# Kernel optimization log

Hardware: AMD Instinct MI355X
Metric: run time of the kernel (lower is better)

## Reference

```python
import jax, jax.numpy as jnp
import numpy as np

S_LEN, BATCH, HID, HEADS = 2048, 4, 1024, 16
HD = HID // HEADS


def setup_inputs() -> dict:
    key = jax.random.key(0)
    ks = jax.random.split(key, 6)

    def lin_w(k, out_dim, in_dim):
        return jax.random.normal(k, (out_dim, in_dim), jnp.float32) * (1.0 / np.sqrt(in_dim))

    return {
        "hidden_states": jax.random.normal(ks[0], (S_LEN, BATCH, HID), jnp.float32),
        "Wq": lin_w(ks[1], HID, HID), "bq": jnp.zeros((HID,), jnp.float32),
        "Wk": lin_w(ks[2], HID, HID), "bk": jnp.zeros((HID,), jnp.float32),
        "Wv": lin_w(ks[3], HID, HID), "bv": jnp.zeros((HID,), jnp.float32),
        "Wf": lin_w(ks[4], HEADS, HID), "bf": jnp.zeros((HEADS,), jnp.float32),
        "Wo": lin_w(ks[5], HID, HID), "bo": jnp.zeros((HID,), jnp.float32),
    }


def _forget_attention(hidden_states, Wq, bq, Wk, bk, Wv, bv, Wf, bf, Wo, bo):
    S, B, H = hidden_states.shape
    nh, hd = HEADS, HD

    def shape(x):
        return x.reshape(S, B, nh, hd)

    q = shape(hidden_states @ Wq.T + bq)
    k = shape(hidden_states @ Wk.T + bk)
    v = shape(hidden_states @ Wv.T + bv)

    # kernel_fn = elu(x) + 1
    phi_q = jax.nn.elu(q) + 1.0
    phi_k = jax.nn.elu(k) + 1.0

    f = jax.nn.sigmoid(hidden_states @ Wf.T + bf)  # [S, B, nh]

    # F_{t,j} = prod_{i=j+1}^{t} f_i  factorizes into the recurrence:
    #   S_t = f_t * S_{t-1} + phi_k_t (x) v_t ;  z_t = f_t * z_{t-1} + phi_k_t
    # out_t = (phi_q_t . S_t) / (phi_q_t . z_t + eps)
    def step(carry, xs):
        Sm, z = carry                      # [B,nh,hd,hd], [B,nh,hd]
        ft, pk, pq, vt = xs                # [B,nh], [B,nh,hd] x3
        fte = ft[..., None]
        Sm = fte[..., None] * Sm + pk[..., :, None] * vt[..., None, :]
        z = fte * z + pk
        num = jnp.einsum('bhd,bhde->bhe', pq, Sm)
        den = jnp.einsum('bhd,bhd->bh', pq, z)[..., None]
        return (Sm, z), num / (den + 1e-6)

    init = (jnp.zeros((B, nh, hd, hd), hidden_states.dtype),
            jnp.zeros((B, nh, hd), hidden_states.dtype))
    _, out = jax.lax.scan(step, init, (f, phi_k, phi_q, v))

    out = out.reshape(S, B, H) @ Wo.T + bo
    return out, f


def reference(hidden_states, Wq, bq, Wk, bk, Wv, bv, Wf, bf, Wo, bo):
    out, f = _forget_attention(hidden_states, Wq, bq, Wk, bk, Wv, bv, Wf, bf, Wo, bo)
    return (out, jnp.zeros_like(out), f)
```

## Files before the change

### kernel.cpp

```cpp
#include <hip/hip_runtime.h>
#include <hip/hip_bf16.h>
#include <math.h>

#define S_LEN 2048
#define BATCH 4
#define HID   1024
#define HEADS 16
#define HD    64
#define SB    (S_LEN*BATCH)
#define CHUNK 64
#define NCHUNK (S_LEN/CHUNK)
#define BH    (BATCH*HEADS)
#define NSTK  3200

typedef __bf16 bf16x8 __attribute__((ext_vector_type(8)));
typedef float  f32x4  __attribute__((ext_vector_type(4)));
typedef unsigned short ushort_t;
typedef unsigned short u16x8 __attribute__((ext_vector_type(8)));
typedef unsigned short u16x4 __attribute__((ext_vector_type(4)));

__device__ __forceinline__ unsigned short f2bf(float x) {
    union { float f; unsigned int u; } un; un.f = x;
    unsigned int u = un.u;
    unsigned int r = (u + 0x7FFFu + ((u >> 16) & 1u)) >> 16;
    return (unsigned short)r;
}
__device__ __forceinline__ float bf2f(unsigned short s) {
    union { unsigned int u; float f; } un; un.u = ((unsigned int)s) << 16;
    return un.f;
}

#define JSW(row, j) ((j) ^ ((((row) >> 3) & 7) << 3))

#define GLL16(src, dst) __builtin_amdgcn_global_load_lds( \
    (const __attribute__((address_space(1))) void*)(src), \
    (__attribute__((address_space(3))) void*)(dst), 16, 0, 0)

#define NXU (SB*HID/4)
#define NW1 (NSTK*HID/4)
#define NW2 (HID*HID/4)
#define NBU (NSTK/4)
#define NTOT (NXU+NW1+NW2+NBU)

__global__ __launch_bounds__(256) void prep_kernel(
    const float* __restrict__ X,  const float* __restrict__ Wq,
    const float* __restrict__ Wk, const float* __restrict__ Wv,
    const float* __restrict__ Wf, const float* __restrict__ Wo,
    const float* __restrict__ bq, const float* __restrict__ bk,
    const float* __restrict__ bv, const float* __restrict__ bf,
    ushort_t* __restrict__ Xb, ushort_t* __restrict__ Wstk,
    ushort_t* __restrict__ Wob, float* __restrict__ bstk)
{
    const int i = blockIdx.x * 256 + threadIdx.x;
    if (i < NXU) {
        float4 v = ((const float4*)X)[i];
        ushort4 o; o.x=f2bf(v.x); o.y=f2bf(v.y); o.z=f2bf(v.z); o.w=f2bf(v.w);
        ((ushort4*)Xb)[i] = o;
    } else if (i < NXU + NW1) {
        const int idx4 = (i - NXU) * 4;
        const int row = idx4 >> 10, col = idx4 & 1023;
        float4 v;
        if      (row < 1024) v = *(const float4*)(Wq + (size_t)row*HID + col);
        else if (row < 2048) v = *(const float4*)(Wk + (size_t)(row-1024)*HID + col);
        else if (row < 3072) v = *(const float4*)(Wv + (size_t)(row-2048)*HID + col);
        else if (row < 3088) v = *(const float4*)(Wf + (size_t)(row-3072)*HID + col);
        else                 v = make_float4(0.f,0.f,0.f,0.f);
        ushort4 o; o.x=f2bf(v.x); o.y=f2bf(v.y); o.z=f2bf(v.z); o.w=f2bf(v.w);
        *(ushort4*)(Wstk + idx4) = o;
    } else if (i < NXU + NW1 + NW2) {
        const int idx4 = (i - NXU - NW1) * 4;
        float4 v = *(const float4*)(Wo + idx4);
        ushort4 o; o.x=f2bf(v.x); o.y=f2bf(v.y); o.z=f2bf(v.z); o.w=f2bf(v.w);
        *(ushort4*)(Wob + idx4) = o;
    } else if (i < NTOT) {
        const int idx4 = (i - NXU - NW1 - NW2) * 4;
        #pragma unroll
        for (int t = 0; t < 4; ++t) {
            const int c = idx4 + t;
            float v;
            if      (c < 1024) v = bq[c];
            else if (c < 2048) v = bk[c-1024];
            else if (c < 3072) v = bv[c-2048];
            else if (c < 3088) v = bf[c-3072];
            else               v = 0.f;
            bstk[c] = v;
        }
    }
}

__global__ __launch_bounds__(256) void qkvf_gemm(
    const ushort_t* __restrict__ X, const ushort_t* __restrict__ W,
    const float* __restrict__ bias,
    ushort_t* __restrict__ Q, ushort_t* __restrict__ Kr,
    ushort_t* __restrict__ V,
    float* __restrict__ f_out, float* __restrict__ logf_out)
{
    __shared__ ushort_t As[128 * 32];
    __shared__ ushort_t Bs[128 * 32];

    const int tid  = threadIdx.x;
    const int wave = tid >> 6, lane = tid & 63;
    const int waveM = wave >> 1, waveN = wave & 1;
    const int rowBase = blockIdx.x * 128;
    const int colBase = blockIdx.y * 128;
    const int K = HID;

    f32x4 acc[4][4];
    #pragma unroll
    for (int i = 0; i < 4; ++i)
        #pragma unroll
        for (int j = 0; j < 4; ++j)
            acc[i][j] = (f32x4){0.f, 0.f, 0.f, 0.f};

    const int srow = lane >> 2;
    const int scol = (lane & 3) * 8;

    const ushort_t* gA0 = X + (size_t)(rowBase + wave*16 + srow) * K + scol;
    const ushort_t* gB0 = W + (size_t)(colBase + wave*16 + srow) * K + scol;
    ushort_t* lA = As + (wave*16)*32;
    ushort_t* lB = Bs + (wave*16)*32;

    const int fr = lane & 15;
    const int fk = (lane >> 4) * 8;

    for (int k0 = 0; k0 < K; k0 += 32) {
        GLL16(gA0 + k0,                lA);
        GLL16(gA0 + (size_t)64*K + k0, lA + 64*32);
        GLL16(gB0 + k0,                lB);
        GLL16(gB0 + (size_t)64*K + k0, lB + 64*32);

        __syncthreads();

        bf16x8 a[4], b[4];
        #pragma unroll
        for (int i = 0; i < 4; ++i)
            a[i] = *(const bf16x8*)(As + (waveM*64 + i*16 + fr)*32 + fk);
        #pragma unroll
        for (int j = 0; j < 4; ++j)
            b[j] = *(const bf16x8*)(Bs + (waveN*64 + j*16 + fr)*32 + fk);

        #pragma unroll
        for (int i = 0; i < 4; ++i)
            #pragma unroll
            for (int j = 0; j < 4; ++j)
                acc[i][j] = __builtin_amdgcn_mfma_f32_16x16x32_bf16(
                    a[i], b[j], acc[i][j], 0, 0, 0);

        __syncthreads();
    }

    const int er = (lane >> 4) * 4;
    const int ec = lane & 15;
    #pragma unroll
    for (int i = 0; i < 4; ++i) {
        #pragma unroll
        for (int j = 0; j < 4; ++j) {
            const int r0 = rowBase + waveM*64 + i*16 + er;
            const int c0 = colBase + waveN*64 + j*16;
            if (c0 >= 3088) continue;
            const int c  = c0 + ec;
            const float bv = bias[c];
            #pragma unroll
            for (int k = 0; k < 4; ++k) {
                float v = acc[i][j][k] + bv;
                const int r = r0 + k;
                if (c0 < 1024) {
                    v = (v > 0.f) ? (v + 1.f) : __expf(v);
                    Q[(size_t)r * HID + c] = f2bf(v);
                } else if (c0 < 2048) {
                    v = (v > 0.f) ? (v + 1.f) : __expf(v);
                    Kr[(size_t)r * HID + (c - 1024)] = f2bf(v);
                } else if (c0 < 3072) {
                    V[(size_t)r * HID + (c - 2048)] = f2bf(v);
                } else {
                    const int n = c - 3072;
                    const float fv = 1.f / (1.f + __expf(-v));
                    f_out[(size_t)r * HEADS + n]    = fv;
                    logf_out[(size_t)r * HEADS + n] = -__logf(1.f + __expf(-v));
                }
            }
        }
    }
}

__global__ __launch_bounds__(256) void gemm_out(
    const ushort_t* __restrict__ X, const ushort_t* __restrict__ W,
    const float* __restrict__ bias, float* __restrict__ Y)
{
    __shared__ ushort_t As[128 * 32];
    __shared__ ushort_t Bs[128 * 32];

    const int tid  = threadIdx.x;
    const int wave = tid >> 6, lane = tid & 63;
    const int waveM = wave >> 1, waveN = wave & 1;
    const int rowBase = blockIdx.x * 128;
    const int colBase = blockIdx.y * 128;
    const int K = HID, N = HID;

    f32x4 acc[4][4];
    #pragma unroll
    for (int i = 0; i < 4; ++i)
        #pragma unroll
        for (int j = 0; j < 4; ++j)
            acc[i][j] = (f32x4){0.f, 0.f, 0.f, 0.f};

    const int srow = lane >> 2;
    const int scol = (lane & 3) * 8;

    const ushort_t* gA0 = X + (size_t)(rowBase + wave*16 + srow) * K + scol;
    const ushort_t* gB0 = W + (size_t)(colBase + wave*16 + srow) * K + scol;
    ushort_t* lA = As + (wave*16)*32;
    ushort_t* lB = Bs + (wave*16)*32;

    const int fr = lane & 15;
    const int fk = (lane >> 4) * 8;

    for (int k0 = 0; k0 < K; k0 += 32) {
        GLL16(gA0 + k0,                lA);
        GLL16(gA0 + (size_t)64*K + k0, lA + 64*32);
        GLL16(gB0 + k0,                lB);
        GLL16(gB0 + (size_t)64*K + k0, lB + 64*32);

        __syncthreads();

        bf16x8 a[4], b[4];
        #pragma unroll
        for (int i = 0; i < 4; ++i)
            a[i] = *(const bf16x8*)(As + (waveM*64 + i*16 + fr)*32 + fk);
        #pragma unroll
        for (int j = 0; j < 4; ++j)
            b[j] = *(const bf16x8*)(Bs + (waveN*64 + j*16 + fr)*32 + fk);

        #pragma unroll
        for (int i = 0; i < 4; ++i)
            #pragma unroll
            for (int j = 0; j < 4; ++j)
                acc[i][j] = __builtin_amdgcn_mfma_f32_16x16x32_bf16(
                    a[i], b[j], acc[i][j], 0, 0, 0);

        __syncthreads();
    }

    const int er = (lane >> 4) * 4;
    const int ec = lane & 15;
    #pragma unroll
    for (int i = 0; i < 4; ++i) {
        #pragma unroll
        for (int j = 0; j < 4; ++j) {
            const int r0 = rowBase + waveM*64 + i*16 + er;
            const int c  = colBase + waveN*64 + j*16 + ec;
            const float bv = bias[c];
            #pragma unroll
            for (int k = 0; k < 4; ++k) {
                const size_t off = (size_t)(r0 + k) * N + c;
                Y[off] = acc[i][j][k] + bv;
            }
        }
    }
}

__global__ __launch_bounds__(256) void pass1_kernel(
    const ushort_t* __restrict__ Kp, const ushort_t* __restrict__ Vp,
    const float* __restrict__ logf,
    ushort_t* __restrict__ Schunk, float* __restrict__ zchunk,
    float* __restrict__ Dchunk)
{
    __shared__ __align__(16) char smem[18688];
    ushort_t* vsT = (ushort_t*)smem;
    ushort_t* kTd = (ushort_t*)(smem + 9216);
    float*    exd = (float*)(smem + 18432);

    const int chunk = blockIdx.x;
    const int bh = blockIdx.y;
    const int b = bh >> 4, h = bh & 15;
    const int tid = threadIdx.x;
    const int wv = tid >> 6, ln = tid & 63;
    const int fr = ln & 15, q4 = ln >> 4;
    const size_t slot = (size_t)bh * NCHUNK + chunk;

    u16x8 vreg[2], kreg[2];
    #pragma unroll
    for (int it = 0; it < 2; ++it) {
        const int u = it*256 + tid;
        const int j = u >> 3, d8 = (u & 7) * 8;
        const size_t base = (size_t)((chunk*64 + j)*BATCH + b)*HID + h*HD + d8;
        vreg[it] = *(const u16x8*)(Vp + base);
        kreg[it] = *(const u16x8*)(Kp + base);
    }
    if (tid < 64) {
        float v = logf[(size_t)((chunk*64 + tid)*BATCH + b) * HEADS + h];
        #pragma unroll
        for (int off = 1; off < 64; off <<= 1) {
            float n = __shfl_up(v, off);
            if (tid >= off) v += n;
        }
        const float tot = __shfl(v, 63);
        exd[tid] = __expf(tot - v);
        if (tid == 63) Dchunk[slot] = __expf(tot);
    }
    __syncthreads();

    #pragma unroll
    for (int it = 0; it < 2; ++it) {
        const int u = it*256 + tid;
        const int j = u >> 3, d8 = (u & 7) * 8;
        const int js = j ^ ((u & 7) << 3);
        const float ex = exd[j];
        #pragma unroll
        for (int i = 0; i < 8; ++i) {
            vsT[(d8+i)*72 + js] = vreg[it][i];
            kTd[(d8+i)*72 + js] = f2bf(bf2f(kreg[it][i]) * ex);
        }
    }
    __syncthreads();

    f32x4 acc[4];
    #pragma unroll
    for (int nt = 0; nt < 4; ++nt) acc[nt] = (f32x4){0.f,0.f,0.f,0.f};
    #pragma unroll
    for (int k0 = 0; k0 < 64; k0 += 32) {
        const int rA = wv*16 + fr;
        bf16x8 av = *(const bf16x8*)(vsT + rA*72 + JSW(rA, k0 + q4*8));
        #pragma unroll
        for (int nt = 0; nt < 4; ++nt) {
            const int rB = nt*16 + fr;
            bf16x8 bk = *(const bf16x8*)(kTd + rB*72 + JSW(rB, k0 + q4*8));
            acc[nt] = __builtin_amdgcn_mfma_f32_16x16x32_bf16(av, bk, acc[nt], 0, 0, 0);
        }
    }

    if (wv == 0) {
        u16x8 onesu;
        #pragma unroll
        for (int i = 0; i < 8; ++i) onesu[i] = 0x3F80;
        const bf16x8 ones = *(const bf16x8*)&onesu;
        f32x4 zacc[4];
        #pragma unroll
        for (int nt = 0; nt < 4; ++nt) zacc[nt] = (f32x4){0.f,0.f,0.f,0.f};
        #pragma unroll
        for (int k0 = 0; k0 < 64; k0 += 32) {
            #pragma unroll
            for (int nt = 0; nt < 4; ++nt) {
                const int rB = nt*16 + fr;
                bf16x8 bk = *(const bf16x8*)(kTd + rB*72 + JSW(rB, k0 + q4*8));
                zacc[nt] = __builtin_amdgcn_mfma_f32_16x16x32_bf16(ones, bk, zacc[nt], 0, 0, 0);
            }
        }
        if (q4 == 0) {
            #pragma unroll
            for (int nt = 0; nt < 4; ++nt)
                zchunk[slot*64 + nt*16 + fr] = zacc[nt][0];
        }
    }

    ushort_t* sp = Schunk + slot * 4096;
    #pragma unroll
    for (int nt = 0; nt < 4; ++nt) {
        #pragma unroll
        for (int r = 0; r < 4; ++r) {
            const int e = wv*16 + q4*4 + r;
            sp[e*64 + nt*16 + fr] = f2bf(acc[nt][r]);
        }
    }
}

__global__ __launch_bounds__(128) void pass2_kernel(
    ushort_t* __restrict__ Schunk, float* __restrict__ zchunk,
    const float* __restrict__ Dchunk)
{
    __shared__ float Ds[NCHUNK];
    const int bh  = blockIdx.x >> 3;
    const int sl  = blockIdx.x & 7;
    const int tid = threadIdx.x;

    if (tid < NCHUNK) Ds[tid] = Dchunk[bh * NCHUNK + tid];

    float Sprev[4] = {0.f, 0.f, 0.f, 0.f};
    float zprev = 0.f;

    const size_t base  = (size_t)bh * NCHUNK * 4096 + sl * 512 + tid * 4;
    const size_t zbase = (size_t)bh * NCHUNK * 64;
    const bool doZ = (sl == 0) && (tid < 64);

    u16x4 b0 = *(const u16x4*)(Schunk + base);
    u16x4 b1 = *(const u16x4*)(Schunk + base + 4096);
    float z0v = 0.f, z1v = 0.f;
    if (doZ) {
        z0v = zchunk[zbase + tid];
        z1v = zchunk[zbase + 64 + tid];
    }
    __syncthreads();

    for (int c = 0; c < NCHUNK; ++c) {
        const float D = Ds[c];
        ushort_t* sp = Schunk + base + (size_t)c * 4096;
        u16x4 wout;
        #pragma unroll
        for (int i = 0; i < 4; ++i) {
            wout[i] = f2bf(Sprev[i]);
            Sprev[i] = D * Sprev[i] + bf2f(b0[i]);
        }
        *(u16x4*)sp = wout;
        b0 = b1;
        if (doZ) {
            zchunk[zbase + (size_t)c * 64 + tid] = zprev;
            zprev = D * zprev + z0v;
            z0v = z1v;
        }
        if (c + 2 < NCHUNK) {
            b1 = *(const u16x4*)(Schunk + base + (size_t)(c+2)*4096);
            if (doZ) z1v = zchunk[zbase + (size_t)(c+2)*64 + tid];
        }
    }
}

__global__ __launch_bounds__(256) void pass3_kernel(
    const ushort_t* __restrict__ Qp, const ushort_t* __restrict__ Kp,
    const ushort_t* __restrict__ Vp, const float* __restrict__ logf,
    const ushort_t* __restrict__ S0, const float* __restrict__ z0,
    ushort_t* __restrict__ AO)
{
    __shared__ __align__(16) char smem[28928];
    ushort_t* qs  = (ushort_t*)smem;
    ushort_t* ks  = (ushort_t*)(smem + 9216);
    ushort_t* vsT = (ushort_t*)(smem + 9216);
    ushort_t* psA = (ushort_t*)(smem + 18432);
    float* cc  = (float*)(smem + 27648);
    float* exT = (float*)(smem + 27904);
    float* qz  = (float*)(smem + 28160);
    float* den = (float*)(smem + 28416);
    float* zz  = (float*)(smem + 28672);

    const int chunk = blockIdx.x;
    const int bh = blockIdx.y;
    const int b = bh >> 4, h = bh & 15;
    const int tid = threadIdx.x;
    const int wv = tid >> 6, ln = tid & 63;
    const int fr = ln & 15, q4 = ln >> 4;
    const size_t slot = (size_t)bh * NCHUNK + chunk;

    u16x8 vreg[2];
    #pragma unroll
    for (int it = 0; it < 2; ++it) {
        const int u = it*256 + tid;
        const int j = u >> 3, d8 = (u & 7) * 8;
        vreg[it] = *(const u16x8*)(Vp + (size_t)((chunk*64 + j)*BATCH + b)*HID + h*HD + d8);
    }

    if (tid < 64) {
        zz[tid] = z0[slot * 64 + tid];
        float v = logf[(size_t)((chunk*64 + tid)*BATCH + b) * HEADS + h];
        #pragma unroll
        for (int off = 1; off < 64; off <<= 1) {
            float n = __shfl_up(v, off);
            if (tid >= off) v += n;
        }
        cc[tid]  = v;
        exT[tid] = __expf(v);
    }
    #pragma unroll
    for (int it = 0; it < 2; ++it) {
        const int u = it*256 + tid;
        const int r = u >> 3, c8 = (u & 7) * 8;
        const size_t goff = (size_t)((chunk*64 + r)*BATCH + b) * HID + h*HD + c8;
        *(u16x8*)(qs + r*72 + c8) = *(const u16x8*)(Qp + goff);
        *(u16x8*)(ks + r*72 + c8) = *(const u16x8*)(Kp + goff);
    }
    __syncthreads();

    f32x4 pacc[4];
    #pragma unroll
    for (int nt = 0; nt < 4; ++nt) pacc[nt] = (f32x4){0.f,0.f,0.f,0.f};
    #pragma unroll
    for (int k0 = 0; k0 < 64; k0 += 32) {
        bf16x8 af = *(const bf16x8*)(qs + (wv*16 + fr)*72 + k0 + q4*8);
        #pragma unroll
        for (int nt = 0; nt < 4; ++nt) {
            bf16x8 bfr = *(const bf16x8*)(ks + (nt*16 + fr)*72 + k0 + q4*8);
            pacc[nt] = __builtin_amdgcn_mfma_f32_16x16x32_bf16(af, bfr, pacc[nt], 0, 0, 0);
        }
    }
    {
        const int t = wv*16 + fr;
        const int d0 = q4 * 16;
        float s = 0.f;
        #pragma unroll
        for (int i = 0; i < 16; ++i)
            s += bf2f(qs[t*72 + d0 + i]) * zz[d0 + i];
        s += __shfl_xor(s, 16);
        s += __shfl_xor(s, 32);
        if (q4 == 0) qz[t] = s;
    }
    __syncthreads();

    #pragma unroll
    for (int it = 0; it < 2; ++it) {
        const int u = it*256 + tid;
        const int j = u >> 3, d8 = (u & 7) * 8;
        const int js = j ^ ((u & 7) << 3);
        #pragma unroll
        for (int i = 0; i < 8; ++i)
            vsT[(d8+i)*72 + js] = vreg[it][i];
    }
    {
        float rs[4] = {0.f, 0.f, 0.f, 0.f};
        float cct[4];
        #pragma unroll
        for (int r = 0; r < 4; ++r) cct[r] = cc[wv*16 + q4*4 + r];
        #pragma unroll
        for (int nt = 0; nt < 4; ++nt) {
            const int j = nt*16 + fr;
            const float ccj = cc[j];
            #pragma unroll
            for (int r = 0; r < 4; ++r) {
                const int t = wv*16 + q4*4 + r;
                float p = (j <= t) ? pacc[nt][r] * __expf(cct[r] - ccj) : 0.f;
                rs[r] += p;
                psA[t*72 + j] = f2bf(p);
            }
        }
        #pragma unroll
        for (int m = 1; m < 16; m <<= 1) {
            #pragma unroll
            for (int r = 0; r < 4; ++r) rs[r] += __shfl_xor(rs[r], m);
        }
        if (fr == 0) {
            #pragma unroll
            for (int r = 0; r < 4; ++r) {
                const int t = wv*16 + q4*4 + r;
                den[t] = rs[r] + exT[t] * qz[t] + 1e-6f;
            }
        }
    }
    __syncthreads();

    f32x4 oacc[4], oacc2[4];
    #pragma unroll
    for (int nt = 0; nt < 4; ++nt) {
        oacc[nt]  = (f32x4){0.f,0.f,0.f,0.f};
        oacc2[nt] = (f32x4){0.f,0.f,0.f,0.f};
    }
    const ushort_t* S0p = S0 + slot * 4096;
    #pragma unroll
    for (int k0 = 0; k0 < 64; k0 += 32) {
        const int k8 = k0 + q4*8;
        bf16x8 ap = *(const bf16x8*)(psA + (wv*16 + fr)*72 + k8);
        bf16x8 aq = *(const bf16x8*)(qs  + (wv*16 + fr)*72 + k8);
        #pragma unroll
        for (int nt = 0; nt < 4; ++nt) {
            const int rV = nt*16 + fr;
            bf16x8 bv = *(const bf16x8*)(vsT + rV*72 + JSW(rV, k8));
            oacc[nt] = __builtin_amdgcn_mfma_f32_16x16x32_bf16(ap, bv, oacc[nt], 0, 0, 0);
            bf16x8 sb = *(const bf16x8*)(S0p + rV*64 + k8);
            oacc2[nt] = __builtin_amdgcn_mfma_f32_16x16x32_bf16(aq, sb, oacc2[nt], 0, 0, 0);
        }
    }
    #pragma unroll
    for (int nt = 0; nt < 4; ++nt) {
        const int e = nt*16 + fr;
        #pragma unroll
        for (int r = 0; r < 4; ++r) {
            const int t = wv*16 + q4*4 + r;
            const float v = (oacc[nt][r] + exT[t] * oacc2[nt][r]) / den[t];
            AO[(size_t)((chunk*64 + t)*BATCH + b) * HID + h*HD + e] = f2bf(v);
        }
    }
}

extern "C" void kernel_launch(void* const* d_in, const int* in_sizes, int n_in,
                              void* d_out, int out_size, void* d_ws, size_t ws_size,
                              hipStream_t stream) {
    const float* X  = (const float*)d_in[0];
    const float* Wq = (const float*)d_in[1];
    const float* bq = (const float*)d_in[2];
    const float* Wk = (const float*)d_in[3];
    const float* bk = (const float*)d_in[4];
    const float* Wv = (const float*)d_in[5];
    const float* bv = (const float*)d_in[6];
    const float* Wf = (const float*)d_in[7];
    const float* bf = (const float*)d_in[8];
    const float* Wo = (const float*)d_in[9];
    const float* bo = (const float*)d_in[10];

    float* out = (float*)d_out;
    const size_t OUT_SLOT = (size_t)SB * HID;

    char* ws = (char*)d_ws;
    ushort_t* wsXb   = (ushort_t*)ws;
    ushort_t* wsWstk = wsXb + (size_t)SB * HID;
    ushort_t* wsWob  = wsWstk + (size_t)NSTK * HID;
    ushort_t* wsQ    = wsWob + (size_t)HID * HID;
    ushort_t* wsK    = wsQ + (size_t)SB * HID;
    ushort_t* wsV    = wsK + (size_t)SB * HID;
    float* wsBstk = (float*)(wsV + (size_t)SB * HID);
    float* wsLogf = wsBstk + NSTK;
    ushort_t* wsS  = (ushort_t*)(wsLogf + (size_t)SB * HEADS);
    float* wsZ    = (float*)(wsS + (size_t)BH * NCHUNK * HD * HD);
    float* wsD    = wsZ + (size_t)BH * NCHUNK * HD;

    hipMemsetAsync(out + OUT_SLOT, 0, OUT_SLOT * sizeof(float), stream);

    prep_kernel<<<(NTOT + 255)/256, 256, 0, stream>>>(
        X, Wq, Wk, Wv, Wf, Wo, bq, bk, bv, bf,
        wsXb, wsWstk, wsWob, wsBstk);

    dim3 qgrid(SB/128, NSTK/128);
    qkvf_gemm<<<qgrid, 256, 0, stream>>>(
        wsXb, wsWstk, wsBstk, wsQ, wsK, wsV,
        out + 2*OUT_SLOT, wsLogf);

    dim3 sgrid(NCHUNK, BH);
    pass1_kernel<<<sgrid, 256, 0, stream>>>(wsK, wsV, wsLogf, wsS, wsZ, wsD);
    pass2_kernel<<<BH*8, 128, 0, stream>>>(wsS, wsZ, wsD);
    pass3_kernel<<<sgrid, 256, 0, stream>>>(wsQ, wsK, wsV, wsLogf, wsS, wsZ, wsXb);

    dim3 ogrid(SB/128, HID/128);
    gemm_out<<<ogrid, 256, 0, stream>>>(wsXb, wsWob, bo, out);
}
```

Before: 284.3 us.

## Load GEMM fragments directly from global memory with register double-buffering

Both projection GEMMs stop staging A/B tiles through LDS with global_load_lds and barriers. Each lane now loads its MFMA operand fragments straight from global memory, prefetching the next k-step into registers while the current MFMAs run. This removes the LDS round-trip and the two __syncthreads per k-step. In exchange, global traffic becomes redundant because waves sharing rows or columns each load the same data, leaning on L2 and cache, and register pressure rises.

After: 437.1 us. +53.7%, slower.

```diff
diff --git a/kernel.cpp b/kernel.cpp
--- a/kernel.cpp
+++ b/kernel.cpp
@@ -31,10 +31,6 @@
 }
 
 #define JSW(row, j) ((j) ^ ((((row) >> 3) & 7) << 3))
-
-#define GLL16(src, dst) __builtin_amdgcn_global_load_lds( \
-    (const __attribute__((address_space(1))) void*)(src), \
-    (__attribute__((address_space(3))) void*)(dst), 16, 0, 0)
 
 #define NXU (SB*HID/4)
 #define NW1 (NSTK*HID/4)
@@ -95,15 +91,14 @@
     ushort_t* __restrict__ V,
     float* __restrict__ f_out, float* __restrict__ logf_out)
 {
-    __shared__ ushort_t As[128 * 32];
-    __shared__ ushort_t Bs[128 * 32];
-
     const int tid  = threadIdx.x;
     const int wave = tid >> 6, lane = tid & 63;
     const int waveM = wave >> 1, waveN = wave & 1;
     const int rowBase = blockIdx.x * 128;
     const int colBase = blockIdx.y * 128;
     const int K = HID;
+    const int fr = lane & 15;
+    const int fk = (lane >> 4) * 8;
 
     f32x4 acc[4][4];
     #pragma unroll
@@ -112,41 +107,38 @@
         for (int j = 0; j < 4; ++j)
             acc[i][j] = (f32x4){0.f, 0.f, 0.f, 0.f};
 
-    const int srow = lane >> 2;
-    const int scol = (lane & 3) * 8;
-
-    const ushort_t* gA0 = X + (size_t)(rowBase + wave*16 + srow) * K + scol;
-    const ushort_t* gB0 = W + (size_t)(colBase + wave*16 + srow) * K + scol;
-    ushort_t* lA = As + (wave*16)*32;
-    ushort_t* lB = Bs + (wave*16)*32;
-
-    const int fr = lane & 15;
-    const int fk = (lane >> 4) * 8;
-
+    const ushort_t* gA[4];
+    const ushort_t* gB[4];
+    #pragma unroll
+    for (int i = 0; i < 4; ++i) {
+        gA[i] = X + (size_t)(rowBase + waveM*64 + i*16 + fr) * K + fk;
+        gB[i] = W + (size_t)(colBase + waveN*64 + i*16 + fr) * K + fk;
+    }
+
+    bf16x8 aC[4], bC[4], aN[4], bN[4];
+    #pragma unroll
+    for (int i = 0; i < 4; ++i) {
+        aC[i] = *(const bf16x8*)(gA[i]);
+        bC[i] = *(const bf16x8*)(gB[i]);
+    }
+
+    #pragma unroll 2
     for (int k0 = 0; k0 < K; k0 += 32) {
-        GLL16(gA0 + k0,                lA);
-        GLL16(gA0 + (size_t)64*K + k0, lA + 64*32);
-        GLL16(gB0 + k0,                lB);
-        GLL16(gB0 + (size_t)64*K + k0, lB + 64*32);
-
-        __syncthreads();
-
-        bf16x8 a[4], b[4];
-        #pragma unroll
-        for (int i = 0; i < 4; ++i)
-            a[i] = *(const bf16x8*)(As + (waveM*64 + i*16 + fr)*32 + fk);
-        #pragma unroll
-        for (int j = 0; j < 4; ++j)
-            b[j] = *(const bf16x8*)(Bs + (waveN*64 + j*16 + fr)*32 + fk);
-
+        if (k0 + 32 < K) {
+            #pragma unroll
+            for (int i = 0; i < 4; ++i) {
+                aN[i] = *(const bf16x8*)(gA[i] + k0 + 32);
+                bN[i] = *(const bf16x8*)(gB[i] + k0 + 32);
+            }
+        }
         #pragma unroll
         for (int i = 0; i < 4; ++i)
             #pragma unroll
             for (int j = 0; j < 4; ++j)
                 acc[i][j] = __builtin_amdgcn_mfma_f32_16x16x32_bf16(
-                    a[i], b[j], acc[i][j], 0, 0, 0);
-
-        __syncthreads();
+                    aC[i], bC[j], acc[i][j], 0, 0, 0);
+        #pragma unroll
+        for (int i = 0; i < 4; ++i) { aC[i] = aN[i]; bC[i] = bN[i]; }
     }
 
     const int er = (lane >> 4) * 4;
@@ -187,15 +179,14 @@
     const ushort_t* __restrict__ X, const ushort_t* __restrict__ W,
     const float* __restrict__ bias, float* __restrict__ Y)
 {
-    __shared__ ushort_t As[128 * 32];
-    __shared__ ushort_t Bs[128 * 32];
-
     const int tid  = threadIdx.x;
     const int wave = tid >> 6, lane = tid & 63;
     const int waveM = wave >> 1, waveN = wave & 1;
     const int rowBase = blockIdx.x * 128;
     const int colBase = blockIdx.y * 128;
     const int K = HID, N = HID;
+    const int fr = lane & 15;
+    const int fk = (lane >> 4) * 8;
 
     f32x4 acc[4][4];
     #pragma unroll
@@ -204,41 +195,38 @@
         for (int j = 0; j < 4; ++j)
             acc[i][j] = (f32x4){0.f, 0.f, 0.f, 0.f};
 
-    const int srow = lane >> 2;
-    const int scol = (lane & 3) * 8;
-
-    const ushort_t* gA0 = X + (size_t)(rowBase + wave*16 + srow) * K + scol;
-    const ushort_t* gB0 = W + (size_t)(colBase + wave*16 + srow) * K + scol;
-    ushort_t* lA = As + (wave*16)*32;
-    ushort_t* lB = Bs + (wave*16)*32;
-
-    const int fr = lane & 15;
-    const int fk = (lane >> 4) * 8;
-
+    const ushort_t* gA[4];
+    const ushort_t* gB[4];
+    #pragma unroll
+    for (int i = 0; i < 4; ++i) {
+        gA[i] = X + (size_t)(rowBase + waveM*64 + i*16 + fr) * K + fk;
+        gB[i] = W + (size_t)(colBase + waveN*64 + i*16 + fr) * K + fk;
+    }
+
+    bf16x8 aC[4], bC[4], aN[4], bN[4];
+    #pragma unroll
+    for (int i = 0; i < 4; ++i) {
+        aC[i] = *(const bf16x8*)(gA[i]);
+        bC[i] = *(const bf16x8*)(gB[i]);
+    }
+
+    #pragma unroll 2
     for (int k0 = 0; k0 < K; k0 += 32) {
-        GLL16(gA0 + k0,                lA);
-        GLL16(gA0 + (size_t)64*K + k0, lA + 64*32);
-        GLL16(gB0 + k0,                lB);
-        GLL16(gB0 + (size_t)64*K + k0, lB + 64*32);
-
-        __syncthreads();
-
-        bf16x8 a[4], b[4];
-        #pragma unroll
-        for (int i = 0; i < 4; ++i)
-            a[i] = *(const bf16x8*)(As + (waveM*64 + i*16 + fr)*32 + fk);
-        #pragma unroll
-        for (int j = 0; j < 4; ++j)
-            b[j] = *(const bf16x8*)(Bs + (waveN*64 + j*16 + fr)*32 + fk);
-
+        if (k0 + 32 < K) {
+            #pragma unroll
+            for (int i = 0; i < 4; ++i) {
+                aN[i] = *(const bf16x8*)(gA[i] + k0 + 32);
+                bN[i] = *(const bf16x8*)(gB[i] + k0 + 32);
+            }
+        }
         #pragma unroll
         for (int i = 0; i < 4; ++i)
             #pragma unroll
             for (int j = 0; j < 4; ++j)
                 acc[i][j] = __builtin_amdgcn_mfma_f32_16x16x32_bf16(
-                    a[i], b[j], acc[i][j], 0, 0, 0);
-
-        __syncthreads();
+                    aC[i], bC[j], acc[i][j], 0, 0, 0);
+        #pragma unroll
+        for (int i = 0; i < 4; ++i) { aC[i] = aN[i]; bC[i] = bN[i]; }
     }
 
     const int er = (lane >> 4) * 4;
```
